# Optimization experiments

Measured on AMD Instinct MI355X. Metric: run time of the kernel, lower is better.

Reference implementation:

```python
import jax, jax.numpy as jnp
import numpy as np


def setup_inputs() -> dict:
    key = jax.random.key(0)
    k = jax.random.split(key, 6)
    E, F_len, B, r = 64, 128, 1024, 16
    E2 = E * E
    hid = max(1, E2 // r)
    return {
        "mu": jax.random.normal(k[0], (5, B, E, F_len), dtype=jnp.float32),
        "A": jax.random.uniform(k[1], (E, E), dtype=jnp.float32),
        "W1": jax.random.normal(k[2], (hid, E2), dtype=jnp.float32) * 0.02,
        "W2": jax.random.normal(k[3], (E2, hid), dtype=jnp.float32) * 0.02,
        "T1": jax.random.normal(k[4], (5, F_len, F_len), dtype=jnp.float32) * 0.01,
        "T2": jax.random.normal(k[5], (5, F_len, F_len), dtype=jnp.float32) * 0.01,
    }


def reference(mu, A, W1, W2, T1, T2):
    E = A.shape[0]
    # dynamic adjacency: squeeze-excite on flattened A (Linear has no bias)
    h = jax.nn.elu(A.reshape(-1) @ W1.T)          # [E2//r]
    Ad = jax.nn.relu(h @ W2.T).reshape(E, E)       # [E, E]
    # diag(1/rowsum) @ Ad == row-wise normalization (same math, O(E^2))
    D_invA = Ad / jnp.maximum(Ad.sum(axis=1, keepdims=True), 1e-6)
    # per-band chain, vectorized over the 5 bands: elu(D_invA @ elu(m @ T1) @ T2)
    h1 = jax.nn.elu(jnp.einsum('gbef,gfh->gbeh', mu, T1))   # [5,B,E,F]
    h2 = jnp.einsum('xe,gbeh->gbxh', D_invA, h1)            # [5,B,E,F]
    out = jax.nn.elu(jnp.einsum('gbeh,ghf->gbef', h2, T2))  # [5,B,E,F]
    return out
```

## Files before the change

kernel.cpp:

```cpp
#include <hip/hip_runtime.h>
#include <hip/hip_bf16.h>
#include <math.h>

typedef short bf16x8 __attribute__((ext_vector_type(8)));
typedef float f32x4 __attribute__((ext_vector_type(4)));
typedef float float4v __attribute__((ext_vector_type(4)));
typedef unsigned short ushort4v __attribute__((ext_vector_type(4)));

static __device__ __forceinline__ float eluf(float x) {
  float e = __expf(x) - 1.0f;
  return x > 0.f ? x : e;
}
static __device__ __forceinline__ unsigned short f2bf(float f) {
  __hip_bfloat16 h = __float2bfloat16(f);
  return *reinterpret_cast<unsigned short*>(&h);
}
static __device__ __forceinline__ unsigned short f2bf_rne(float f) {
  union { float f; unsigned u; } v; v.f = f;
  unsigned r = v.u + 0x7FFFu + ((v.u >> 16) & 1u);
  return (unsigned short)(r >> 16);
}

__global__ void k_hidden(const float* __restrict__ A, const float* __restrict__ W1,
                         float* __restrict__ hout) {
  int j = blockIdx.x, t = threadIdx.x;
  const float* row = W1 + (size_t)j * 4096;
  float s = 0.f;
  for (int i = t; i < 4096; i += 256) s += A[i] * row[i];
  __shared__ float red[256];
  red[t] = s; __syncthreads();
  for (int off = 128; off > 0; off >>= 1) {
    if (t < off) red[t] += red[t + off];
    __syncthreads();
  }
  if (t == 0) {
    float x = red[0];
    hout[j] = x > 0.f ? x : expm1f(x);
  }
}

__global__ void k_dinv(const float* __restrict__ hbuf, const float* __restrict__ W2,
                       unsigned short* __restrict__ Dout) {
  int x = blockIdx.x, t = threadIdx.x;
  int lane = t & 63, w = t >> 6;
  __shared__ float hs[256];
  __shared__ float ad[64];
  hs[t] = hbuf[t];
  __syncthreads();
  for (int ei = 0; ei < 16; ++ei) {
    int e = w * 16 + ei;
    const float* row = W2 + (size_t)(x * 64 + e) * 256;
    float p = 0.f;
    for (int q = 0; q < 4; ++q) p += row[q * 64 + lane] * hs[q * 64 + lane];
    for (int off = 32; off > 0; off >>= 1) p += __shfl_down(p, off);
    if (lane == 0) ad[e] = fmaxf(p, 0.f);
  }
  __syncthreads();
  if (t < 64) {
    float v = ad[t];
    float rs = v;
    for (int off = 1; off < 64; off <<= 1) rs += __shfl_xor(rs, off);
    Dout[x * 64 + t] = f2bf_rne(v / fmaxf(rs, 1e-6f));
  }
}

__global__ void k_transT(const float* __restrict__ T1, const float* __restrict__ T2,
                         unsigned short* __restrict__ T1T, unsigned short* __restrict__ T2T) {
  int idx = blockIdx.x * 256 + threadIdx.x;
  const float* src = (idx < 81920) ? T1 : T2;
  unsigned short* dst = (idx < 81920) ? T1T : T2T;
  int o = (idx < 81920) ? idx : idx - 81920;
  int g = o >> 14;
  int r = o & 16383;
  int h = r >> 7;
  int f = r & 127;
  dst[o] = f2bf_rne(src[g * 16384 + f * 128 + h]);
}

__launch_bounds__(256, 3)
__global__ void k_main(const float* __restrict__ mu,
                       const unsigned short* __restrict__ Dm,
                       const unsigned short* __restrict__ T1T,
                       const unsigned short* __restrict__ T2T,
                       float* __restrict__ out) {
  __shared__ __align__(16) char smem[32768];
  char* s_mu = smem;
  char* s_h1 = smem + 16384;
  char* s_h2 = smem;

  const int g = blockIdx.y, b = blockIdx.x;
  const int t = threadIdx.x;
  const int lane = t & 63, w = t >> 6;
  const int l15 = lane & 15, lk = lane >> 4;
  const int nb = w * 32;

  const float* mub = mu + (size_t)(g * 1024 + b) * 8192;
  float4v v[8];
  #pragma unroll
  for (int k = 0; k < 8; ++k) v[k] = ((const float4v*)mub)[t + k * 256];

  const unsigned short* t1g = T1T + g * 16384;
  bf16x8 tb0[4], tb1[4];
  #pragma unroll
  for (int kc = 0; kc < 4; ++kc) {
    int k0 = kc * 32 + lk * 8;
    tb0[kc] = *(const bf16x8*)(const void*)(t1g + (nb + l15) * 128 + k0);
    tb1[kc] = *(const bf16x8*)(const void*)(t1g + (nb + 16 + l15) * 128 + k0);
  }
  bf16x8 aDf[4][2];
  #pragma unroll
  for (int m = 0; m < 4; ++m)
    #pragma unroll
    for (int kc = 0; kc < 2; ++kc)
      aDf[m][kc] = *(const bf16x8*)(const void*)(Dm + (m * 16 + l15) * 64 + kc * 32 + lk * 8);

  #pragma unroll
  for (int k = 0; k < 8; ++k) {
    int q = t + k * 256;
    int row = q >> 5;
    int col4 = (q & 31) * 4;
    ushort4v u;
    u[0] = f2bf(v[k][0]); u[1] = f2bf(v[k][1]); u[2] = f2bf(v[k][2]); u[3] = f2bf(v[k][3]);
    int byte = (row * 256 + col4 * 2) ^ ((row & 7) << 4);
    *(ushort4v*)(s_mu + byte) = u;
  }
  __syncthreads();

  f32x4 acc[4][2];
  #pragma unroll
  for (int m = 0; m < 4; ++m)
    #pragma unroll
    for (int n = 0; n < 2; ++n)
      acc[m][n] = (f32x4){0.f, 0.f, 0.f, 0.f};

  #pragma unroll
  for (int kc = 0; kc < 4; ++kc) {
    int k0 = kc * 32 + lk * 8;
    #pragma unroll
    for (int m = 0; m < 4; ++m) {
      int row = m * 16 + l15;
      int byte = (row * 256 + k0 * 2) ^ ((row & 7) << 4);
      bf16x8 a = *(const bf16x8*)(s_mu + byte);
      acc[m][0] = __builtin_amdgcn_mfma_f32_16x16x32_bf16(a, tb0[kc], acc[m][0], 0, 0, 0);
      acc[m][1] = __builtin_amdgcn_mfma_f32_16x16x32_bf16(a, tb1[kc], acc[m][1], 0, 0, 0);
    }
  }
  const unsigned short* t2g = T2T + g * 16384;
  bf16x8 t2b0[4], t2b1[4];
  #pragma unroll
  for (int kc = 0; kc < 4; ++kc) {
    int k0 = kc * 32 + lk * 8;
    t2b0[kc] = *(const bf16x8*)(const void*)(t2g + (nb + l15) * 128 + k0);
    t2b1[kc] = *(const bf16x8*)(const void*)(t2g + (nb + 16 + l15) * 128 + k0);
  }
  #pragma unroll
  for (int m = 0; m < 4; ++m)
    #pragma unroll
    for (int n = 0; n < 2; ++n) {
      int col = nb + n * 16 + l15;
      int e0 = m * 16 + lk * 4;
      ushort4v u;
      u[0] = f2bf(eluf(acc[m][n][0]));
      u[1] = f2bf(eluf(acc[m][n][1]));
      u[2] = f2bf(eluf(acc[m][n][2]));
      u[3] = f2bf(eluf(acc[m][n][3]));
      int byte = (col * 128 + e0 * 2) ^ ((col & 7) << 4);
      *(ushort4v*)(s_h1 + byte) = u;
    }
  __syncthreads();

  f32x4 acc2[4][2];
  #pragma unroll
  for (int m = 0; m < 4; ++m)
    #pragma unroll
    for (int n = 0; n < 2; ++n)
      acc2[m][n] = (f32x4){0.f, 0.f, 0.f, 0.f};

  #pragma unroll
  for (int kc = 0; kc < 2; ++kc) {
    int k0 = kc * 32 + lk * 8;
    int c0 = nb + l15, c1 = nb + 16 + l15;
    bf16x8 b0 = *(const bf16x8*)(s_h1 + ((c0 * 128 + k0 * 2) ^ ((c0 & 7) << 4)));
    bf16x8 b1 = *(const bf16x8*)(s_h1 + ((c1 * 128 + k0 * 2) ^ ((c1 & 7) << 4)));
    #pragma unroll
    for (int m = 0; m < 4; ++m) {
      acc2[m][0] = __builtin_amdgcn_mfma_f32_16x16x32_bf16(aDf[m][kc], b0, acc2[m][0], 0, 0, 0);
      acc2[m][1] = __builtin_amdgcn_mfma_f32_16x16x32_bf16(aDf[m][kc], b1, acc2[m][1], 0, 0, 0);
    }
  }
  #pragma unroll
  for (int m = 0; m < 4; ++m)
    #pragma unroll
    for (int n = 0; n < 2; ++n) {
      int hc = nb + n * 16 + l15;
      #pragma unroll
      for (int r = 0; r < 4; ++r) {
        int x = m * 16 + lk * 4 + r;
        int byte = (x * 256 + hc * 2) ^ ((x & 7) << 4);
        *(unsigned short*)(s_h2 + byte) = f2bf(acc2[m][n][r]);
      }
    }
  __syncthreads();

  f32x4 acc3[4][2];
  #pragma unroll
  for (int m = 0; m < 4; ++m)
    #pragma unroll
    for (int n = 0; n < 2; ++n)
      acc3[m][n] = (f32x4){0.f, 0.f, 0.f, 0.f};

  #pragma unroll
  for (int kc = 0; kc < 4; ++kc) {
    int k0 = kc * 32 + lk * 8;
    #pragma unroll
    for (int m = 0; m < 4; ++m) {
      int row = m * 16 + l15;
      int byte = (row * 256 + k0 * 2) ^ ((row & 7) << 4);
      bf16x8 a = *(const bf16x8*)(s_h2 + byte);
      acc3[m][0] = __builtin_amdgcn_mfma_f32_16x16x32_bf16(a, t2b0[kc], acc3[m][0], 0, 0, 0);
      acc3[m][1] = __builtin_amdgcn_mfma_f32_16x16x32_bf16(a, t2b1[kc], acc3[m][1], 0, 0, 0);
    }
  }
  float* ob = out + (size_t)(g * 1024 + b) * 8192;
  #pragma unroll
  for (int m = 0; m < 4; ++m)
    #pragma unroll
    for (int n = 0; n < 2; ++n) {
      int f = nb + n * 16 + l15;
      #pragma unroll
      for (int r = 0; r < 4; ++r) {
        int e = m * 16 + lk * 4 + r;
        ob[e * 128 + f] = eluf(acc3[m][n][r]);
      }
    }
}

extern "C" void kernel_launch(void* const* d_in, const int* in_sizes, int n_in,
                              void* d_out, int out_size, void* d_ws, size_t ws_size,
                              hipStream_t stream) {
  const float* mu = (const float*)d_in[0];
  const float* A  = (const float*)d_in[1];
  const float* W1 = (const float*)d_in[2];
  const float* W2 = (const float*)d_in[3];
  const float* T1 = (const float*)d_in[4];
  const float* T2 = (const float*)d_in[5];
  float* out = (float*)d_out;

  char* ws = (char*)d_ws;
  float* hbuf          = (float*)ws;
  unsigned short* Dm   = (unsigned short*)(ws + 1024);
  unsigned short* T1T  = (unsigned short*)(ws + 9216);
  unsigned short* T2T  = (unsigned short*)(ws + 173056);

  hipLaunchKernelGGL(k_hidden, dim3(256), dim3(256), 0, stream, A, W1, hbuf);
  hipLaunchKernelGGL(k_dinv,   dim3(64),  dim3(256), 0, stream, hbuf, W2, Dm);
  hipLaunchKernelGGL(k_transT, dim3(640), dim3(256), 0, stream, T1, T2, T1T, T2T);
  hipLaunchKernelGGL(k_main,   dim3(1024, 5), dim3(256), 0, stream, mu, Dm, T1T, T2T, out);
}
```

Baseline: 122.3 us.

## Process four batches per block with double-buffered mu prefetch and merged prep kernels

```diff
diff --git a/kernel.cpp b/kernel.cpp
--- a/kernel.cpp
+++ b/kernel.cpp
@@ -39,200 +39,206 @@
   }
 }
 
-__global__ void k_dinv(const float* __restrict__ hbuf, const float* __restrict__ W2,
-                       unsigned short* __restrict__ Dout) {
-  int x = blockIdx.x, t = threadIdx.x;
-  int lane = t & 63, w = t >> 6;
-  __shared__ float hs[256];
-  __shared__ float ad[64];
-  hs[t] = hbuf[t];
-  __syncthreads();
-  for (int ei = 0; ei < 16; ++ei) {
-    int e = w * 16 + ei;
-    const float* row = W2 + (size_t)(x * 64 + e) * 256;
-    float p = 0.f;
-    for (int q = 0; q < 4; ++q) p += row[q * 64 + lane] * hs[q * 64 + lane];
-    for (int off = 32; off > 0; off >>= 1) p += __shfl_down(p, off);
-    if (lane == 0) ad[e] = fmaxf(p, 0.f);
-  }
-  __syncthreads();
-  if (t < 64) {
-    float v = ad[t];
-    float rs = v;
-    for (int off = 1; off < 64; off <<= 1) rs += __shfl_xor(rs, off);
-    Dout[x * 64 + t] = f2bf_rne(v / fmaxf(rs, 1e-6f));
-  }
-}
-
-__global__ void k_transT(const float* __restrict__ T1, const float* __restrict__ T2,
-                         unsigned short* __restrict__ T1T, unsigned short* __restrict__ T2T) {
-  int idx = blockIdx.x * 256 + threadIdx.x;
-  const float* src = (idx < 81920) ? T1 : T2;
-  unsigned short* dst = (idx < 81920) ? T1T : T2T;
-  int o = (idx < 81920) ? idx : idx - 81920;
-  int g = o >> 14;
-  int r = o & 16383;
-  int h = r >> 7;
-  int f = r & 127;
-  dst[o] = f2bf_rne(src[g * 16384 + f * 128 + h]);
-}
-
-__launch_bounds__(256, 3)
+__global__ void k_pre2(const float* __restrict__ hbuf, const float* __restrict__ W2,
+                       unsigned short* __restrict__ Dout,
+                       const float* __restrict__ T1, const float* __restrict__ T2,
+                       unsigned short* __restrict__ T1T, unsigned short* __restrict__ T2T) {
+  int t = threadIdx.x;
+  if (blockIdx.x < 64) {
+    int x = blockIdx.x;
+    int lane = t & 63, w = t >> 6;
+    __shared__ float hs[256];
+    __shared__ float ad[64];
+    hs[t] = hbuf[t];
+    __syncthreads();
+    for (int ei = 0; ei < 16; ++ei) {
+      int e = w * 16 + ei;
+      const float* row = W2 + (size_t)(x * 64 + e) * 256;
+      float p = 0.f;
+      for (int q = 0; q < 4; ++q) p += row[q * 64 + lane] * hs[q * 64 + lane];
+      for (int off = 32; off > 0; off >>= 1) p += __shfl_down(p, off);
+      if (lane == 0) ad[e] = fmaxf(p, 0.f);
+    }
+    __syncthreads();
+    if (t < 64) {
+      float v = ad[t];
+      float rs = v;
+      for (int off = 1; off < 64; off <<= 1) rs += __shfl_xor(rs, off);
+      Dout[x * 64 + t] = f2bf_rne(v / fmaxf(rs, 1e-6f));
+    }
+  } else {
+    int idx = (blockIdx.x - 64) * 256 + t;
+    const float* src = (idx < 81920) ? T1 : T2;
+    unsigned short* dst = (idx < 81920) ? T1T : T2T;
+    int o = (idx < 81920) ? idx : idx - 81920;
+    int g = o >> 14;
+    int r = o & 16383;
+    int h = r >> 7;
+    int f = r & 127;
+    dst[o] = f2bf_rne(src[g * 16384 + f * 128 + h]);
+  }
+}
+
+__launch_bounds__(256, 2)
 __global__ void k_main(const float* __restrict__ mu,
                        const unsigned short* __restrict__ Dm,
                        const unsigned short* __restrict__ T1T,
                        const unsigned short* __restrict__ T2T,
                        float* __restrict__ out) {
-  __shared__ __align__(16) char smem[32768];
-  char* s_mu = smem;
-  char* s_h1 = smem + 16384;
-  char* s_h2 = smem;
-
-  const int g = blockIdx.y, b = blockIdx.x;
+  __shared__ __align__(16) char smem[49152];
+  char* s_h1 = smem + 32768;
+
+  const int g = blockIdx.y, b0 = blockIdx.x * 4;
   const int t = threadIdx.x;
   const int lane = t & 63, w = t >> 6;
   const int l15 = lane & 15, lk = lane >> 4;
   const int nb = w * 32;
 
-  const float* mub = mu + (size_t)(g * 1024 + b) * 8192;
-  float4v v[8];
-  #pragma unroll
-  for (int k = 0; k < 8; ++k) v[k] = ((const float4v*)mub)[t + k * 256];
-
   const unsigned short* t1g = T1T + g * 16384;
-  bf16x8 tb0[4], tb1[4];
+  const unsigned short* t2g = T2T + g * 16384;
+  bf16x8 tb0[4], tb1[4], t2b0[4], t2b1[4];
   #pragma unroll
   for (int kc = 0; kc < 4; ++kc) {
     int k0 = kc * 32 + lk * 8;
-    tb0[kc] = *(const bf16x8*)(const void*)(t1g + (nb + l15) * 128 + k0);
-    tb1[kc] = *(const bf16x8*)(const void*)(t1g + (nb + 16 + l15) * 128 + k0);
+    tb0[kc]  = *(const bf16x8*)(const void*)(t1g + (nb + l15) * 128 + k0);
+    tb1[kc]  = *(const bf16x8*)(const void*)(t1g + (nb + 16 + l15) * 128 + k0);
+    t2b0[kc] = *(const bf16x8*)(const void*)(t2g + (nb + l15) * 128 + k0);
+    t2b1[kc] = *(const bf16x8*)(const void*)(t2g + (nb + 16 + l15) * 128 + k0);
   }
   bf16x8 aDf[4][2];
   #pragma unroll
-  for (int m = 0; m < 4; ++m)
+  for (int np = 0; np < 4; ++np)
     #pragma unroll
     for (int kc = 0; kc < 2; ++kc)
-      aDf[m][kc] = *(const bf16x8*)(const void*)(Dm + (m * 16 + l15) * 64 + kc * 32 + lk * 8);
-
-  #pragma unroll
-  for (int k = 0; k < 8; ++k) {
-    int q = t + k * 256;
-    int row = q >> 5;
-    int col4 = (q & 31) * 4;
-    ushort4v u;
-    u[0] = f2bf(v[k][0]); u[1] = f2bf(v[k][1]); u[2] = f2bf(v[k][2]); u[3] = f2bf(v[k][3]);
-    int byte = (row * 256 + col4 * 2) ^ ((row & 7) << 4);
-    *(ushort4v*)(s_mu + byte) = u;
+      aDf[np][kc] = *(const bf16x8*)(const void*)(Dm + (np * 16 + l15) * 64 + kc * 32 + lk * 8);
+
+  {
+    const float4v* src = (const float4v*)(mu + (size_t)(g * 1024 + b0) * 8192);
+    #pragma unroll
+    for (int k = 0; k < 8; ++k) {
+      int q = t + k * 256;
+      float4v v = src[q];
+      int row = q >> 5, col4 = (q & 31) * 4;
+      ushort4v u;
+      u[0] = f2bf(v[0]); u[1] = f2bf(v[1]); u[2] = f2bf(v[2]); u[3] = f2bf(v[3]);
+      *(ushort4v*)(smem + ((row * 256 + col4 * 2) ^ ((row & 7) << 4))) = u;
+    }
   }
   __syncthreads();
 
-  f32x4 acc[4][2];
-  #pragma unroll
-  for (int m = 0; m < 4; ++m)
-    #pragma unroll
-    for (int n = 0; n < 2; ++n)
-      acc[m][n] = (f32x4){0.f, 0.f, 0.f, 0.f};
-
-  #pragma unroll
-  for (int kc = 0; kc < 4; ++kc) {
-    int k0 = kc * 32 + lk * 8;
-    #pragma unroll
-    for (int m = 0; m < 4; ++m) {
-      int row = m * 16 + l15;
-      int byte = (row * 256 + k0 * 2) ^ ((row & 7) << 4);
-      bf16x8 a = *(const bf16x8*)(s_mu + byte);
-      acc[m][0] = __builtin_amdgcn_mfma_f32_16x16x32_bf16(a, tb0[kc], acc[m][0], 0, 0, 0);
-      acc[m][1] = __builtin_amdgcn_mfma_f32_16x16x32_bf16(a, tb1[kc], acc[m][1], 0, 0, 0);
-    }
-  }
-  const unsigned short* t2g = T2T + g * 16384;
-  bf16x8 t2b0[4], t2b1[4];
-  #pragma unroll
-  for (int kc = 0; kc < 4; ++kc) {
-    int k0 = kc * 32 + lk * 8;
-    t2b0[kc] = *(const bf16x8*)(const void*)(t2g + (nb + l15) * 128 + k0);
-    t2b1[kc] = *(const bf16x8*)(const void*)(t2g + (nb + 16 + l15) * 128 + k0);
-  }
-  #pragma unroll
-  for (int m = 0; m < 4; ++m)
-    #pragma unroll
-    for (int n = 0; n < 2; ++n) {
-      int col = nb + n * 16 + l15;
-      int e0 = m * 16 + lk * 4;
-      ushort4v u;
-      u[0] = f2bf(eluf(acc[m][n][0]));
-      u[1] = f2bf(eluf(acc[m][n][1]));
-      u[2] = f2bf(eluf(acc[m][n][2]));
-      u[3] = f2bf(eluf(acc[m][n][3]));
-      int byte = (col * 128 + e0 * 2) ^ ((col & 7) << 4);
-      *(ushort4v*)(s_h1 + byte) = u;
-    }
-  __syncthreads();
-
-  f32x4 acc2[4][2];
-  #pragma unroll
-  for (int m = 0; m < 4; ++m)
-    #pragma unroll
-    for (int n = 0; n < 2; ++n)
-      acc2[m][n] = (f32x4){0.f, 0.f, 0.f, 0.f};
-
-  #pragma unroll
-  for (int kc = 0; kc < 2; ++kc) {
-    int k0 = kc * 32 + lk * 8;
-    int c0 = nb + l15, c1 = nb + 16 + l15;
-    bf16x8 b0 = *(const bf16x8*)(s_h1 + ((c0 * 128 + k0 * 2) ^ ((c0 & 7) << 4)));
-    bf16x8 b1 = *(const bf16x8*)(s_h1 + ((c1 * 128 + k0 * 2) ^ ((c1 & 7) << 4)));
-    #pragma unroll
-    for (int m = 0; m < 4; ++m) {
-      acc2[m][0] = __builtin_amdgcn_mfma_f32_16x16x32_bf16(aDf[m][kc], b0, acc2[m][0], 0, 0, 0);
-      acc2[m][1] = __builtin_amdgcn_mfma_f32_16x16x32_bf16(aDf[m][kc], b1, acc2[m][1], 0, 0, 0);
-    }
-  }
-  #pragma unroll
-  for (int m = 0; m < 4; ++m)
-    #pragma unroll
-    for (int n = 0; n < 2; ++n) {
-      int hc = nb + n * 16 + l15;
-      #pragma unroll
-      for (int r = 0; r < 4; ++r) {
-        int x = m * 16 + lk * 4 + r;
-        int byte = (x * 256 + hc * 2) ^ ((x & 7) << 4);
-        *(unsigned short*)(s_h2 + byte) = f2bf(acc2[m][n][r]);
-      }
-    }
-  __syncthreads();
-
-  f32x4 acc3[4][2];
-  #pragma unroll
-  for (int m = 0; m < 4; ++m)
-    #pragma unroll
-    for (int n = 0; n < 2; ++n)
-      acc3[m][n] = (f32x4){0.f, 0.f, 0.f, 0.f};
-
-  #pragma unroll
-  for (int kc = 0; kc < 4; ++kc) {
-    int k0 = kc * 32 + lk * 8;
-    #pragma unroll
-    for (int m = 0; m < 4; ++m) {
-      int row = m * 16 + l15;
-      int byte = (row * 256 + k0 * 2) ^ ((row & 7) << 4);
-      bf16x8 a = *(const bf16x8*)(s_h2 + byte);
-      acc3[m][0] = __builtin_amdgcn_mfma_f32_16x16x32_bf16(a, t2b0[kc], acc3[m][0], 0, 0, 0);
-      acc3[m][1] = __builtin_amdgcn_mfma_f32_16x16x32_bf16(a, t2b1[kc], acc3[m][1], 0, 0, 0);
-    }
-  }
-  float* ob = out + (size_t)(g * 1024 + b) * 8192;
-  #pragma unroll
-  for (int m = 0; m < 4; ++m)
-    #pragma unroll
-    for (int n = 0; n < 2; ++n) {
-      int f = nb + n * 16 + l15;
-      #pragma unroll
-      for (int r = 0; r < 4; ++r) {
-        int e = m * 16 + lk * 4 + r;
-        ob[e * 128 + f] = eluf(acc3[m][n][r]);
-      }
-    }
+  #pragma unroll 1
+  for (int it = 0; it < 4; ++it) {
+    char* bcur = smem + ((it & 1) << 14);
+    char* bnxt = smem + (((it + 1) & 1) << 14);
+    const bool pre = (it < 3);
+
+    float4v vn[8];
+    if (pre) {
+      const float4v* srcn = (const float4v*)(mu + (size_t)(g * 1024 + b0 + it + 1) * 8192);
+      #pragma unroll
+      for (int k = 0; k < 8; ++k) vn[k] = srcn[t + k * 256];
+      __builtin_amdgcn_sched_barrier(0);
+    }
+
+    f32x4 acc[4][2];
+    #pragma unroll
+    for (int m = 0; m < 4; ++m) { acc[m][0] = (f32x4){0,0,0,0}; acc[m][1] = (f32x4){0,0,0,0}; }
+    #pragma unroll
+    for (int kc = 0; kc < 4; ++kc) {
+      int k0 = kc * 32 + lk * 8;
+      #pragma unroll
+      for (int m = 0; m < 4; ++m) {
+        int row = m * 16 + l15;
+        bf16x8 a = *(const bf16x8*)(bcur + ((row * 256 + k0 * 2) ^ ((row & 7) << 4)));
+        acc[m][0] = __builtin_amdgcn_mfma_f32_16x16x32_bf16(a, tb0[kc], acc[m][0], 0, 0, 0);
+        acc[m][1] = __builtin_amdgcn_mfma_f32_16x16x32_bf16(a, tb1[kc], acc[m][1], 0, 0, 0);
+      }
+    }
+    #pragma unroll
+    for (int m = 0; m < 4; ++m)
+      #pragma unroll
+      for (int n = 0; n < 2; ++n) {
+        int col = nb + n * 16 + l15;
+        int e0 = m * 16 + lk * 4;
+        ushort4v u;
+        u[0] = f2bf(eluf(acc[m][n][0]));
+        u[1] = f2bf(eluf(acc[m][n][1]));
+        u[2] = f2bf(eluf(acc[m][n][2]));
+        u[3] = f2bf(eluf(acc[m][n][3]));
+        *(ushort4v*)(s_h1 + ((col * 128 + e0 * 2) ^ ((col & 7) << 4))) = u;
+      }
+    __syncthreads();
+
+    f32x4 acc2[2][4];
+    #pragma unroll
+    for (int mp = 0; mp < 2; ++mp)
+      #pragma unroll
+      for (int np = 0; np < 4; ++np) acc2[mp][np] = (f32x4){0,0,0,0};
+    #pragma unroll
+    for (int kc = 0; kc < 2; ++kc) {
+      int e0 = kc * 32 + lk * 8;
+      int hr0 = w * 32 + l15, hr1 = w * 32 + 16 + l15;
+      bf16x8 a0 = *(const bf16x8*)(s_h1 + ((hr0 * 128 + e0 * 2) ^ ((hr0 & 7) << 4)));
+      bf16x8 a1 = *(const bf16x8*)(s_h1 + ((hr1 * 128 + e0 * 2) ^ ((hr1 & 7) << 4)));
+      #pragma unroll
+      for (int np = 0; np < 4; ++np) {
+        acc2[0][np] = __builtin_amdgcn_mfma_f32_16x16x32_bf16(a0, aDf[np][kc], acc2[0][np], 0, 0, 0);
+        acc2[1][np] = __builtin_amdgcn_mfma_f32_16x16x32_bf16(a1, aDf[np][kc], acc2[1][np], 0, 0, 0);
+      }
+    }
+    #pragma unroll
+    for (int mp = 0; mp < 2; ++mp)
+      #pragma unroll
+      for (int np = 0; np < 4; ++np) {
+        int x = np * 16 + l15;
+        int h0 = w * 32 + mp * 16 + lk * 4;
+        ushort4v u;
+        u[0] = f2bf(acc2[mp][np][0]);
+        u[1] = f2bf(acc2[mp][np][1]);
+        u[2] = f2bf(acc2[mp][np][2]);
+        u[3] = f2bf(acc2[mp][np][3]);
+        *(ushort4v*)(bcur + ((x * 256 + h0 * 2) ^ ((x & 7) << 4))) = u;
+      }
+    if (pre) {
+      #pragma unroll
+      for (int k = 0; k < 8; ++k) {
+        int q = t + k * 256;
+        int row = q >> 5, col4 = (q & 31) * 4;
+        ushort4v u;
+        u[0] = f2bf(vn[k][0]); u[1] = f2bf(vn[k][1]);
+        u[2] = f2bf(vn[k][2]); u[3] = f2bf(vn[k][3]);
+        *(ushort4v*)(bnxt + ((row * 256 + col4 * 2) ^ ((row & 7) << 4))) = u;
+      }
+    }
+    __syncthreads();
+
+    f32x4 acc3[4][2];
+    #pragma unroll
+    for (int m = 0; m < 4; ++m) { acc3[m][0] = (f32x4){0,0,0,0}; acc3[m][1] = (f32x4){0,0,0,0}; }
+    #pragma unroll
+    for (int kc = 0; kc < 4; ++kc) {
+      int k0 = kc * 32 + lk * 8;
+      #pragma unroll
+      for (int m = 0; m < 4; ++m) {
+        int row = m * 16 + l15;
+        bf16x8 a = *(const bf16x8*)(bcur + ((row * 256 + k0 * 2) ^ ((row & 7) << 4)));
+        acc3[m][0] = __builtin_amdgcn_mfma_f32_16x16x32_bf16(a, t2b0[kc], acc3[m][0], 0, 0, 0);
+        acc3[m][1] = __builtin_amdgcn_mfma_f32_16x16x32_bf16(a, t2b1[kc], acc3[m][1], 0, 0, 0);
+      }
+    }
+    float* ob = out + (size_t)(g * 1024 + b0 + it) * 8192;
+    #pragma unroll
+    for (int m = 0; m < 4; ++m)
+      #pragma unroll
+      for (int n = 0; n < 2; ++n) {
+        int f = nb + n * 16 + l15;
+        #pragma unroll
+        for (int r = 0; r < 4; ++r) {
+          int e = m * 16 + lk * 4 + r;
+          ob[e * 128 + f] = eluf(acc3[m][n][r]);
+        }
+      }
+  }
 }
 
 extern "C" void kernel_launch(void* const* d_in, const int* in_sizes, int n_in,
@@ -253,7 +259,6 @@
   unsigned short* T2T  = (unsigned short*)(ws + 173056);
 
   hipLaunchKernelGGL(k_hidden, dim3(256), dim3(256), 0, stream, A, W1, hbuf);
-  hipLaunchKernelGGL(k_dinv,   dim3(64),  dim3(256), 0, stream, hbuf, W2, Dm);
-  hipLaunchKernelGGL(k_transT, dim3(640), dim3(256), 0, stream, T1, T2, T1T, T2T);
-  hipLaunchKernelGGL(k_main,   dim3(1024, 5), dim3(256), 0, stream, mu, Dm, T1T, T2T, out);
-}
+  hipLaunchKernelGGL(k_pre2,   dim3(704), dim3(256), 0, stream, hbuf, W2, Dm, T1, T2, T1T, T2T);
+  hipLaunchKernelGGL(k_main,   dim3(256, 5), dim3(256), 0, stream, mu, Dm, T1T, T2T, out);
+}
```

Result: faster. 101.5 us (-17.0%).
